# Kernel optimization log

Hardware: AMD Instinct MI355X
Metric: run time of the kernel (lower is better)

The kernel has to match this reference:

```python
import jax, jax.numpy as jnp
import numpy as np

B, S, D_IN, D_OUT = 8, 2048, 512, 512

def setup_inputs() -> dict:
    key = jax.random.key(0)
    ks = jax.random.split(key, 10)
    s = 1.0 / np.sqrt(D_IN)
    return {
        "Q": jax.random.normal(ks[0], (B, S, D_IN), jnp.float32),
        "K": jax.random.normal(ks[1], (B, S, D_IN), jnp.float32),
        "V": jax.random.normal(ks[2], (B, S, D_IN), jnp.float32),
        "attn_mask": jax.random.normal(ks[3], (B, S, S), jnp.float32),
        "Wq": jax.random.normal(ks[4], (D_IN, D_OUT), jnp.float32) * s,
        "bq": jnp.zeros((D_OUT,), jnp.float32),
        "Wk": jax.random.normal(ks[5], (D_IN, D_OUT), jnp.float32) * s,
        "bk": jnp.zeros((D_OUT,), jnp.float32),
        "Wv": jax.random.normal(ks[6], (D_IN, D_OUT), jnp.float32) * s,
        "bv": jnp.zeros((D_OUT,), jnp.float32),
    }

def reference(Q, K, V, attn_mask, Wq, bq, Wk, bk, Wv, bv):
    # separate QKV projections
    q_s = jnp.einsum('bsd,de->bse', Q, Wq) + bq
    k_s = jnp.einsum('bsd,de->bse', K, Wk) + bk
    v_s = jnp.einsum('bsd,de->bse', V, Wv) + bv
    # scaled dot-product; note: source scales by sqrt(d_in)
    scale = 1.0 / np.sqrt(Q.shape[-1]).astype(np.float32)
    scores = jnp.einsum('bqe,bke->bqk', q_s, k_s) * scale + attn_mask
    attn = jax.nn.softmax(scores, axis=-1)
    return jnp.einsum('bqk,bke->bqe', attn, v_s)
```

## Files before the change

### kernel.cpp

```cpp
#include <hip/hip_runtime.h>


typedef __bf16 bf16x8 __attribute__((ext_vector_type(8)));
typedef float f32x4 __attribute__((ext_vector_type(4)));

__device__ inline unsigned short f2bf(float x) {
  union { float f; unsigned u; } c; c.f = x;
  unsigned u = c.u;
  return (unsigned short)((u + 0x7fffu + ((u >> 16) & 1u)) >> 16);
}

__device__ inline void load_lds16(const void* g, void* lds) {
  __builtin_amdgcn_global_load_lds(
      (__attribute__((address_space(1))) void*)(g),
      (__attribute__((address_space(3))) void*)(lds),
      16, 0, 0);
}

__global__ __launch_bounds__(256) void cvt4(const float4* __restrict__ src,
                                            ushort4* __restrict__ dst, int n4) {
  int i = blockIdx.x * 256 + threadIdx.x;
  if (i < n4) {
    float4 f = src[i];
    ushort4 o;
    o.x = f2bf(f.x); o.y = f2bf(f.y); o.z = f2bf(f.z); o.w = f2bf(f.w);
    dst[i] = o;
  }
}

__global__ void wtrans(const float* __restrict__ W, unsigned short* __restrict__ Wt) {
  __shared__ float t[32][33];
  const int x = threadIdx.x, y = threadIdx.y;
  const int n0 = blockIdx.x * 32, k0 = blockIdx.y * 32;
#pragma unroll
  for (int j = 0; j < 32; j += 8) t[y + j][x] = W[(size_t)(k0 + y + j) * 512 + n0 + x];
  __syncthreads();
#pragma unroll
  for (int j = 0; j < 32; j += 8)
    Wt[(size_t)(n0 + y + j) * 512 + k0 + x] = f2bf(t[x][y + j]);
}

enum { EPI_PROJ = 0, EPI_SCORES = 1, EPI_PV = 2 };

template <int EPI>
__global__ __launch_bounds__(256) void gemm_bt(
    const unsigned short* __restrict__ A, size_t sA, int lda,
    const unsigned short* __restrict__ B, size_t sB, int ldb,
    void* __restrict__ Cv, size_t sC, int ldc, int K,
    const float* __restrict__ b0, const float* __restrict__ b1,
    const float* __restrict__ b2, unsigned short* __restrict__ VT,
    const float* __restrict__ mask, float scale, float* __restrict__ Lsum) {
  __shared__ unsigned short As[128 * 32];
  __shared__ unsigned short Bs[128 * 32];

  const int tid = threadIdx.x;
  const int wave = tid >> 6, lane = tid & 63;
  const int z = blockIdx.z;
  const int m0 = blockIdx.y * 128, n0 = blockIdx.x * 128;

  const unsigned short* Ab = A + (size_t)z * sA;
  const unsigned short* Bb = B + (size_t)z * sB;

  const int wr = wave >> 1, wc = wave & 1;
  const int quad = lane >> 4, c16 = lane & 15;
  const int srow = lane >> 2;
  const int schunk = (lane & 3) * 8;

  f32x4 acc[4][4] = {};

  for (int kt = 0; kt < K; kt += 32) {
    __syncthreads();
#pragma unroll
    for (int i = 0; i < 2; ++i) {
      const int inst = wave * 2 + i;
      const int row = inst * 16 + srow;
      load_lds16(Ab + (size_t)(m0 + row) * lda + kt + schunk, &As[inst * 512]);
      load_lds16(Bb + (size_t)(n0 + row) * ldb + kt + schunk, &Bs[inst * 512]);
    }
    __syncthreads();
    bf16x8 af[4], bf[4];
#pragma unroll
    for (int i = 0; i < 4; ++i) {
      af[i] = *(const bf16x8*)&As[(wr * 64 + i * 16 + c16) * 32 + quad * 8];
      bf[i] = *(const bf16x8*)&Bs[(wc * 64 + i * 16 + c16) * 32 + quad * 8];
    }
#pragma unroll
    for (int i = 0; i < 4; ++i)
#pragma unroll
      for (int j = 0; j < 4; ++j)
        acc[i][j] = __builtin_amdgcn_mfma_f32_16x16x32_bf16(af[i], bf[j], acc[i][j], 0, 0, 0);
  }

#pragma unroll
  for (int fr = 0; fr < 4; ++fr) {
    const int rbase = m0 + wr * 64 + fr * 16 + quad * 4;
    if constexpr (EPI == EPI_PROJ) {
#pragma unroll
      for (int fc = 0; fc < 4; ++fc) {
        const int col = n0 + wc * 64 + fc * 16 + c16;
        const float bias = (z == 0 ? b0 : (z == 1 ? b1 : b2))[col];
        if (z < 2) {
          unsigned short* C = (unsigned short*)Cv + (size_t)z * sC;
#pragma unroll
          for (int r = 0; r < 4; ++r)
            C[(size_t)(rbase + r) * ldc + col] = f2bf(acc[fr][fc][r] + bias);
        } else {
          const int b = rbase >> 11, s = rbase & 2047;
          ushort4 p;
          p.x = f2bf(acc[fr][fc][0] + bias);
          p.y = f2bf(acc[fr][fc][1] + bias);
          p.z = f2bf(acc[fr][fc][2] + bias);
          p.w = f2bf(acc[fr][fc][3] + bias);
          *(ushort4*)(VT + ((size_t)b * 512 + col) * 2048 + s) = p;
        }
      }
    } else if constexpr (EPI == EPI_SCORES) {
      unsigned short* P = (unsigned short*)Cv + (size_t)z * sC;
      const float* mb = mask + (size_t)z * 2048 * 2048;
      float rs[4] = {0.f, 0.f, 0.f, 0.f};
#pragma unroll
      for (int fc = 0; fc < 4; ++fc) {
        const int col = n0 + wc * 64 + fc * 16 + c16;
#pragma unroll
        for (int r = 0; r < 4; ++r) {
          const float e = __expf(acc[fr][fc][r] * scale + mb[(size_t)(rbase + r) * 2048 + col]);
          P[(size_t)(rbase + r) * ldc + col] = f2bf(e);
          rs[r] += e;
        }
      }
#pragma unroll
      for (int r = 0; r < 4; ++r) {
#pragma unroll
        for (int off = 1; off < 16; off <<= 1) rs[r] += __shfl_xor(rs[r], off);
      }
      if (c16 == 0) {
#pragma unroll
        for (int r = 0; r < 4; ++r)
          atomicAdd(&Lsum[(size_t)z * 2048 + rbase + r], rs[r]);
      }
    } else {
      float* C = (float*)Cv + (size_t)z * sC;
      float inv[4];
#pragma unroll
      for (int r = 0; r < 4; ++r) inv[r] = 1.0f / Lsum[(size_t)z * 2048 + rbase + r];
#pragma unroll
      for (int fc = 0; fc < 4; ++fc) {
        const int col = n0 + wc * 64 + fc * 16 + c16;
#pragma unroll
        for (int r = 0; r < 4; ++r)
          C[(size_t)(rbase + r) * ldc + col] = acc[fr][fc][r] * inv[r];
      }
    }
  }
}

extern "C" void kernel_launch(void* const* d_in, const int* in_sizes, int n_in,
                              void* d_out, int out_size, void* d_ws, size_t ws_size,
                              hipStream_t stream) {
  const float* Q    = (const float*)d_in[0];
  const float* Kin  = (const float*)d_in[1];
  const float* V    = (const float*)d_in[2];
  const float* mask = (const float*)d_in[3];
  const float* Wq   = (const float*)d_in[4];
  const float* bq   = (const float*)d_in[5];
  const float* Wk   = (const float*)d_in[6];
  const float* bk   = (const float*)d_in[7];
  const float* Wv   = (const float*)d_in[8];
  const float* bv   = (const float*)d_in[9];
  float* out = (float*)d_out;

  const size_t TOKD = (size_t)16384 * 512;

  unsigned short* WT = (unsigned short*)d_ws;
  unsigned short* QS = WT + 3 * 512 * 512;
  unsigned short* KS = QS + TOKD;
  unsigned short* VT = KS + TOKD;
  unsigned short* P  = VT + TOKD;
  float* Lsum = (float*)(P + (size_t)8 * 2048 * 2048);
  unsigned short* QB = (unsigned short*)(Lsum + 16384);

  const float scale = 0.044194173824159216f;

  const int n4 = (int)(TOKD / 4);
  cvt4<<<n4 / 256, 256, 0, stream>>>((const float4*)Q,   (ushort4*)QB, n4);
  cvt4<<<n4 / 256, 256, 0, stream>>>((const float4*)Kin, (ushort4*)(QB + TOKD), n4);
  cvt4<<<n4 / 256, 256, 0, stream>>>((const float4*)V,   (ushort4*)(QB + 2 * TOKD), n4);

  dim3 wtb(32, 8);
  wtrans<<<dim3(16, 16), wtb, 0, stream>>>(Wq, WT);
  wtrans<<<dim3(16, 16), wtb, 0, stream>>>(Wk, WT + 262144);
  wtrans<<<dim3(16, 16), wtb, 0, stream>>>(Wv, WT + 524288);

  hipMemsetAsync(Lsum, 0, 16384 * sizeof(float), stream);

  gemm_bt<EPI_PROJ><<<dim3(4, 128, 3), 256, 0, stream>>>(
      QB, TOKD, 512, WT, 262144, 512, (void*)QS, TOKD, 512, 512,
      bq, bk, bv, VT, nullptr, 0.f, nullptr);

  gemm_bt<EPI_SCORES><<<dim3(16, 16, 8), 256, 0, stream>>>(
      QS, (size_t)2048 * 512, 512,
      KS, (size_t)2048 * 512, 512,
      (void*)P, (size_t)2048 * 2048, 2048, 512,
      nullptr, nullptr, nullptr, nullptr, mask, scale, Lsum);

  gemm_bt<EPI_PV><<<dim3(4, 16, 8), 256, 0, stream>>>(
      P, (size_t)2048 * 2048, 2048,
      VT, (size_t)512 * 2048, 2048,
      (void*)out, (size_t)2048 * 512, 512, 2048,
      nullptr, nullptr, nullptr, nullptr, nullptr, 0.f, Lsum);
}
```

Baseline: 483.0 us.

## Prefetch attention mask into registers during scores GEMM and narrow PV tile

The scores kernel now issues the mask loads for its output tile, spread across the 16 K-iterations and held in 64 registers per thread, so global mask latency overlaps the MFMA main loop instead of stalling the epilogue. The PV GEMM is templated to a 64-wide N tile with twice as many blocks, which raises parallelism for the long-K (2048) GEMM that previously launched only 512 blocks. The cost is much higher register pressure in the scores kernel, which can lower occupancy or cause spills, and smaller per-block reuse in the PV GEMM.

```diff
diff --git a/kernel.cpp b/kernel.cpp
--- a/kernel.cpp
+++ b/kernel.cpp
@@ -42,7 +42,7 @@
 
 enum { EPI_PROJ = 0, EPI_SCORES = 1, EPI_PV = 2 };
 
-template <int EPI>
+template <int EPI, int BN>
 __global__ __launch_bounds__(256) void gemm_bt(
     const unsigned short* __restrict__ A, size_t sA, int lda,
     const unsigned short* __restrict__ B, size_t sB, int ldb,
@@ -50,13 +50,14 @@
     const float* __restrict__ b0, const float* __restrict__ b1,
     const float* __restrict__ b2, unsigned short* __restrict__ VT,
     const float* __restrict__ mask, float scale, float* __restrict__ Lsum) {
+  constexpr int NF = BN / 32;
   __shared__ unsigned short As[128 * 32];
-  __shared__ unsigned short Bs[128 * 32];
+  __shared__ unsigned short Bs[BN * 32];
 
   const int tid = threadIdx.x;
   const int wave = tid >> 6, lane = tid & 63;
   const int z = blockIdx.z;
-  const int m0 = blockIdx.y * 128, n0 = blockIdx.x * 128;
+  const int m0 = blockIdx.y * 128, n0 = blockIdx.x * BN;
 
   const unsigned short* Ab = A + (size_t)z * sA;
   const unsigned short* Bb = B + (size_t)z * sB;
@@ -66,29 +67,62 @@
   const int srow = lane >> 2;
   const int schunk = (lane & 3) * 8;
 
-  f32x4 acc[4][4] = {};
-
-  for (int kt = 0; kt < K; kt += 32) {
-    __syncthreads();
+  f32x4 acc[4][NF] = {};
+  float mreg[EPI == EPI_SCORES ? 64 : 1];
+  const float* mb = (EPI == EPI_SCORES) ? (mask + (size_t)z * 2048 * 2048) : nullptr;
+
+  auto stage = [&](int kt) {
 #pragma unroll
     for (int i = 0; i < 2; ++i) {
       const int inst = wave * 2 + i;
       const int row = inst * 16 + srow;
       load_lds16(Ab + (size_t)(m0 + row) * lda + kt + schunk, &As[inst * 512]);
+    }
+#pragma unroll
+    for (int i = 0; i < BN / 64; ++i) {
+      const int inst = wave * (BN / 64) + i;
+      const int row = inst * 16 + srow;
       load_lds16(Bb + (size_t)(n0 + row) * ldb + kt + schunk, &Bs[inst * 512]);
     }
-    __syncthreads();
-    bf16x8 af[4], bf[4];
-#pragma unroll
-    for (int i = 0; i < 4; ++i) {
+  };
+
+  auto compute = [&]() {
+    bf16x8 af[4], bf[NF];
+#pragma unroll
+    for (int i = 0; i < 4; ++i)
       af[i] = *(const bf16x8*)&As[(wr * 64 + i * 16 + c16) * 32 + quad * 8];
-      bf[i] = *(const bf16x8*)&Bs[(wc * 64 + i * 16 + c16) * 32 + quad * 8];
-    }
+#pragma unroll
+    for (int j = 0; j < NF; ++j)
+      bf[j] = *(const bf16x8*)&Bs[(wc * (BN / 2) + j * 16 + c16) * 32 + quad * 8];
 #pragma unroll
     for (int i = 0; i < 4; ++i)
 #pragma unroll
-      for (int j = 0; j < 4; ++j)
+      for (int j = 0; j < NF; ++j)
         acc[i][j] = __builtin_amdgcn_mfma_f32_16x16x32_bf16(af[i], bf[j], acc[i][j], 0, 0, 0);
+  };
+
+  if constexpr (EPI == EPI_SCORES) {
+#pragma unroll
+    for (int it = 0; it < 16; ++it) {
+      __syncthreads();
+      stage(it * 32);
+#pragma unroll
+      for (int j = 0; j < 4; ++j) {
+        const int idx = it * 4 + j;
+        const int fr = idx >> 4, fc = (idx >> 2) & 3, r = idx & 3;
+        mreg[idx] = mb[(size_t)(m0 + wr * 64 + fr * 16 + quad * 4 + r) * 2048 +
+                       (n0 + wc * 64 + fc * 16 + c16)];
+      }
+      __syncthreads();
+      compute();
+    }
+  } else {
+    for (int kt = 0; kt < K; kt += 32) {
+      __syncthreads();
+      stage(kt);
+      __syncthreads();
+      compute();
+    }
   }
 
 #pragma unroll
@@ -96,8 +130,8 @@
     const int rbase = m0 + wr * 64 + fr * 16 + quad * 4;
     if constexpr (EPI == EPI_PROJ) {
 #pragma unroll
-      for (int fc = 0; fc < 4; ++fc) {
-        const int col = n0 + wc * 64 + fc * 16 + c16;
+      for (int fc = 0; fc < NF; ++fc) {
+        const int col = n0 + wc * (BN / 2) + fc * 16 + c16;
         const float bias = (z == 0 ? b0 : (z == 1 ? b1 : b2))[col];
         if (z < 2) {
           unsigned short* C = (unsigned short*)Cv + (size_t)z * sC;
@@ -116,14 +150,13 @@
       }
     } else if constexpr (EPI == EPI_SCORES) {
       unsigned short* P = (unsigned short*)Cv + (size_t)z * sC;
-      const float* mb = mask + (size_t)z * 2048 * 2048;
       float rs[4] = {0.f, 0.f, 0.f, 0.f};
 #pragma unroll
       for (int fc = 0; fc < 4; ++fc) {
         const int col = n0 + wc * 64 + fc * 16 + c16;
 #pragma unroll
         for (int r = 0; r < 4; ++r) {
-          const float e = __expf(acc[fr][fc][r] * scale + mb[(size_t)(rbase + r) * 2048 + col]);
+          const float e = __expf(acc[fr][fc][r] * scale + mreg[fr * 16 + fc * 4 + r]);
           P[(size_t)(rbase + r) * ldc + col] = f2bf(e);
           rs[r] += e;
         }
@@ -144,8 +177,8 @@
 #pragma unroll
       for (int r = 0; r < 4; ++r) inv[r] = 1.0f / Lsum[(size_t)z * 2048 + rbase + r];
 #pragma unroll
-      for (int fc = 0; fc < 4; ++fc) {
-        const int col = n0 + wc * 64 + fc * 16 + c16;
+      for (int fc = 0; fc < NF; ++fc) {
+        const int col = n0 + wc * (BN / 2) + fc * 16 + c16;
 #pragma unroll
         for (int r = 0; r < 4; ++r)
           C[(size_t)(rbase + r) * ldc + col] = acc[fr][fc][r] * inv[r];
@@ -193,17 +226,17 @@
 
   hipMemsetAsync(Lsum, 0, 16384 * sizeof(float), stream);
 
-  gemm_bt<EPI_PROJ><<<dim3(4, 128, 3), 256, 0, stream>>>(
+  gemm_bt<EPI_PROJ, 128><<<dim3(4, 128, 3), 256, 0, stream>>>(
       QB, TOKD, 512, WT, 262144, 512, (void*)QS, TOKD, 512, 512,
       bq, bk, bv, VT, nullptr, 0.f, nullptr);
 
-  gemm_bt<EPI_SCORES><<<dim3(16, 16, 8), 256, 0, stream>>>(
+  gemm_bt<EPI_SCORES, 128><<<dim3(16, 16, 8), 256, 0, stream>>>(
       QS, (size_t)2048 * 512, 512,
       KS, (size_t)2048 * 512, 512,
       (void*)P, (size_t)2048 * 2048, 2048, 512,
       nullptr, nullptr, nullptr, nullptr, mask, scale, Lsum);
 
-  gemm_bt<EPI_PV><<<dim3(4, 16, 8), 256, 0, stream>>>(
+  gemm_bt<EPI_PV, 64><<<dim3(8, 16, 8), 256, 0, stream>>>(
       P, (size_t)2048 * 2048, 2048,
       VT, (size_t)512 * 2048, 2048,
       (void*)out, (size_t)2048 * 512, 512, 2048,
```

Measured after the change: 481.5 us. Within noise of the previous version (-0.3%).
